# Optimization experiments

Measured on AMD Instinct MI355X. Metric: run time of the kernel, lower is better.

## Reference

```python
import jax, jax.numpy as jnp
import numpy as np
import math

PHI = (1.0 + math.sqrt(5.0)) / 2.0
BASE_FAST = PHI
BASE_SLOW = 1618.0
D = 1024
NH = 16
HD = D // NH
H_GATE = max(8, D // 4)
B, L = 2, 2048


def _rope_cos_sin(seq_len, dim, base):
    # dim assumed even here (D=1024)
    idx = jnp.arange(0, dim, 2, dtype=jnp.float32) / float(dim)
    inv = 1.0 / (base ** idx)
    t = jnp.arange(seq_len, dtype=jnp.float32)
    freqs = jnp.outer(t, inv)                      # (L, dim/2)
    emb = jnp.concatenate([freqs, freqs], axis=-1) # (L, dim)
    return jnp.cos(emb), jnp.sin(emb)


def _rotate_half(x):
    d = x.shape[-1]
    x1, x2 = x[..., : d // 2], x[..., d // 2 :]
    return jnp.concatenate([-x2, x1], axis=-1)


def setup_inputs() -> dict:
    key = jax.random.key(0)
    ks = jax.random.split(key, 16)
    std = 0.02
    inp = {
        "z": jax.random.normal(ks[0], (B, L, D), jnp.float32),
        "pool_seq": jax.random.normal(ks[1], (B, L, D), jnp.float32),
        "Wq": std * jax.random.normal(ks[2], (D, D), jnp.float32),
        "bq": jnp.zeros((D,), jnp.float32),
        "Wk": std * jax.random.normal(ks[3], (D, D), jnp.float32),
        "bk": jnp.zeros((D,), jnp.float32),
        "Wv": std * jax.random.normal(ks[4], (D, D), jnp.float32),
        "bv": jnp.zeros((D,), jnp.float32),
        "W_coh": std * jax.random.normal(ks[5], (D, D), jnp.float32),
        "gamma": jnp.zeros((1,), jnp.float32) + 0.1,  # nonzero so bias path is exercised
        "Wg1": std * jax.random.normal(ks[6], (H_GATE, D), jnp.float32),
        "bg1": jnp.zeros((H_GATE,), jnp.float32),
        "Wg2": std * jax.random.normal(ks[7], (1, H_GATE), jnp.float32),
        "bg2": jnp.zeros((1,), jnp.float32),
    }
    return inp


def reference(z, pool_seq, Wq, bq, Wk, bk, Wv, bv, W_coh, gamma, Wg1, bg1, Wg2, bg2):
    b, l, d = z.shape
    # QKV projections (torch Linear: x @ W^T + b)
    Q = z @ Wq.T + bq
    K_raw = z @ Wk.T + bk
    V = z @ Wv.T + bv

    # Global coherence bias: per-query pool vector dotted with every key
    gk = pool_seq @ W_coh.T                                   # (B,L,D)
    gb = jnp.einsum("bqd,bkd->bqk", gk, K_raw) * (d ** -0.5)  # (B,L,L)
    gb = jnp.tanh(gamma[0]) * gb

    # Per-position RoPE interpolation gate (exact GELU as in torch default)
    h = jax.nn.gelu(pool_seq @ Wg1.T + bg1, approximate=False)
    gate = jax.nn.sigmoid(h @ Wg2.T + bg2)                    # (B,L,1)

    cos_f, sin_f = _rope_cos_sin(l, d, BASE_FAST)             # (L,D)
    cos_s, sin_s = _rope_cos_sin(l, d, BASE_SLOW)
    cos = gate * cos_f + (1.0 - gate) * cos_s                 # (B,L,D)
    sin = gate * sin_f + (1.0 - gate) * sin_s

    Q = Q * cos + _rotate_half(Q) * sin
    K_rot = K_raw * cos + _rotate_half(K_raw) * sin

    nh, hd = NH, d // NH
    Q_h = Q.reshape(b, l, nh, hd).transpose(0, 2, 1, 3)       # (B,H,L,hd)
    K_h = K_rot.reshape(b, l, nh, hd).transpose(0, 2, 1, 3)
    V_h = V.reshape(b, l, nh, hd).transpose(0, 2, 1, 3)

    logits = jnp.einsum("bhqd,bhkd->bhqk", Q_h, K_h) * (hd ** -0.5)
    logits = logits + gb[:, None]                             # broadcast over heads

    causal = jnp.tril(jnp.ones((l, l), dtype=bool))
    logits = jnp.where(causal[None, None], logits, -jnp.inf)

    attn_w_h = jax.nn.softmax(logits, axis=-1)                # (B,H,L,L)
    out_h = jnp.einsum("bhqk,bhkd->bhqd", attn_w_h, V_h)
    out = out_h.transpose(0, 2, 1, 3).reshape(b, l, d)
    attn_w = attn_w_h.mean(axis=1)                            # (B,L,L)
    return out, attn_w
```

## Files before the change

kernel.cpp:

```cpp
#include <hip/hip_runtime.h>
#include <hip/hip_bf16.h>

constexpr int Bn  = 2;
constexpr int Ln  = 2048;
constexpr int Dn  = 1024;
constexpr int NH  = 16;
constexpr int HGn = 256;
constexpr long BLD = (long)Bn * Ln * Dn;

typedef float f32x4 __attribute__((ext_vector_type(4)));
typedef float f32x2 __attribute__((ext_vector_type(2)));
typedef short s16x8 __attribute__((ext_vector_type(8)));
typedef short s16x4 __attribute__((ext_vector_type(4)));
typedef short s16x2 __attribute__((ext_vector_type(2)));

#define DEVI static __device__ __forceinline__

DEVI float bf2f(short u) {
  union { float f; unsigned int i; } v; v.i = ((unsigned int)(unsigned short)u) << 16; return v.f;
}
DEVI short f2bf(float f) {
  union { float f; unsigned int i; } v; v.f = f;
  unsigned int r = v.i + 0x7FFFu + ((v.i >> 16) & 1u);
  return (short)(r >> 16);
}
DEVI void gl_lds16(const void* g, void* l) {
  __builtin_amdgcn_global_load_lds((const __attribute__((address_space(1))) unsigned int*)g,
                                   (__attribute__((address_space(3))) unsigned int*)l, 16, 0, 0);
}

struct CastDesc { const float* src[7]; long cum[8]; };
__global__ void k_cast7(CastDesc d, short* __restrict__ dst) {
  long gi = ((long)blockIdx.x * 256 + threadIdx.x) * 4;
  int s = 0;
#pragma unroll
  for (int i = 1; i < 7; ++i) if (gi >= d.cum[i]) s = i;
  const float* sp = d.src[s] + (gi - d.cum[s]);
  f32x4 v = *(const f32x4*)sp;
  s16x4 o; o[0] = f2bf(v[0]); o[1] = f2bf(v[1]); o[2] = f2bf(v[2]); o[3] = f2bf(v[3]);
  *(s16x4*)(dst + gi) = o;
}

__global__ __launch_bounds__(256)
void k_gemm_mega(const short* __restrict__ zb, const short* __restrict__ pb,
                 const short* __restrict__ Wcat,
                 const float* __restrict__ bq, const float* __restrict__ bk,
                 const float* __restrict__ bv, const float* __restrict__ bg1,
                 short* __restrict__ Qp, short* __restrict__ Kp,
                 short* __restrict__ Vtb, short* __restrict__ Gk,
                 float* __restrict__ Hf) {
  int m0 = blockIdx.y * 128, n0 = blockIdx.x * 128;
  const short* Ap = (n0 < 3072) ? zb : pb;
  __shared__ short smA[128 * 32];
  __shared__ short smB[128 * 32];
  int tid = threadIdx.x;
  int lane = tid & 63, wid = tid >> 6;
  int wr = wid >> 1, wc = wid & 1;
  int lr = lane & 15, lg = lane >> 4;
  int r_in = lane >> 2, c_in = (lane & 3) * 8;
  f32x4 acc[4][4] = {};
  for (int k0 = 0; k0 < Dn; k0 += 32) {
#pragma unroll
    for (int i = 0; i < 2; ++i) {
      int row = wid * 32 + i * 16 + r_in;
      gl_lds16(Ap + (long)(m0 + row) * Dn + k0 + c_in, smA + row * 32 + c_in);
      gl_lds16(Wcat + (long)(n0 + row) * Dn + k0 + c_in, smB + row * 32 + c_in);
    }
    __syncthreads();
    s16x8 af[4], bf[4];
#pragma unroll
    for (int m = 0; m < 4; m++) af[m] = *(const s16x8*)(smA + (wr * 64 + m * 16 + lr) * 32 + lg * 8);
#pragma unroll
    for (int n = 0; n < 4; n++) bf[n] = *(const s16x8*)(smB + (wc * 64 + n * 16 + lr) * 32 + lg * 8);
#pragma unroll
    for (int m = 0; m < 4; m++)
#pragma unroll
      for (int n = 0; n < 4; n++)
        acc[m][n] = __builtin_amdgcn_mfma_f32_16x16x32_bf16(af[m], bf[n], acc[m][n], 0, 0, 0);
    __syncthreads();
  }
  int slice = n0 >> 10;
#pragma unroll
  for (int n = 0; n < 4; n++) {
    int col = n0 + wc * 64 + n * 16 + lr;
    int c = col - (slice << 10);
    float bias = (slice == 0) ? bq[c] : (slice == 1) ? bk[c] : (slice == 2) ? bv[c]
               : (slice == 3) ? 0.0f : bg1[c];
#pragma unroll
    for (int m = 0; m < 4; m++) {
#pragma unroll
      for (int r = 0; r < 4; r++) {
        long row = m0 + wr * 64 + m * 16 + lg * 4 + r;
        float v = acc[m][n][r] + bias;
        if (slice == 4) {
          v = 0.5f * v * (1.0f + erff(v * 0.70710678118f));
          Hf[row * HGn + c] = v;
        } else if (slice == 2) {
          long off = (((row >> 11) * (long)NH + (c >> 6)) * 64 + (c & 63)) * Ln + (row & (Ln - 1));
          Vtb[off] = f2bf(v);
        } else {
          short* dst = (slice == 0) ? Qp : (slice == 1) ? Kp : Gk;
          dst[row * (long)Dn + c] = f2bf(v);
        }
      }
    }
  }
}

__global__ __launch_bounds__(256)
void k_gemm_gb(const short* __restrict__ A, const short* __restrict__ B,
               const float* __restrict__ gamma, short* __restrict__ C) {
  int bz = blockIdx.z;
  const short* Ap = A + (long)bz * Ln * Dn;
  const short* Bp = B + (long)bz * Ln * Dn;
  int m0 = blockIdx.y * 128, n0 = blockIdx.x * 128;
  if (n0 > m0 + 127) return;
  __shared__ short smA[128 * 32];
  __shared__ short smB[128 * 32];
  int tid = threadIdx.x;
  int lane = tid & 63, wid = tid >> 6;
  int wr = wid >> 1, wc = wid & 1;
  int lr = lane & 15, lg = lane >> 4;
  int r_in = lane >> 2, c_in = (lane & 3) * 8;
  f32x4 acc[4][4] = {};
  for (int k0 = 0; k0 < Dn; k0 += 32) {
#pragma unroll
    for (int i = 0; i < 2; ++i) {
      int row = wid * 32 + i * 16 + r_in;
      gl_lds16(Ap + (long)(m0 + row) * Dn + k0 + c_in, smA + row * 32 + c_in);
      gl_lds16(Bp + (long)(n0 + row) * Dn + k0 + c_in, smB + row * 32 + c_in);
    }
    __syncthreads();
    s16x8 af[4], bf[4];
#pragma unroll
    for (int m = 0; m < 4; m++) af[m] = *(const s16x8*)(smA + (wr * 64 + m * 16 + lr) * 32 + lg * 8);
#pragma unroll
    for (int n = 0; n < 4; n++) bf[n] = *(const s16x8*)(smB + (wc * 64 + n * 16 + lr) * 32 + lg * 8);
#pragma unroll
    for (int m = 0; m < 4; m++)
#pragma unroll
      for (int n = 0; n < 4; n++)
        acc[m][n] = __builtin_amdgcn_mfma_f32_16x16x32_bf16(af[m], bf[n], acc[m][n], 0, 0, 0);
    __syncthreads();
  }
  float alpha = tanhf(gamma[0]) * 0.03125f;
#pragma unroll
  for (int n = 0; n < 4; n++) {
    int col = n0 + wc * 64 + n * 16 + lr;
#pragma unroll
    for (int m = 0; m < 4; m++) {
#pragma unroll
      for (int r = 0; r < 4; r++) {
        long row = m0 + wr * 64 + m * 16 + lg * 4 + r;
        C[(long)bz * Ln * Ln + row * Ln + col] = f2bf(acc[m][n][r] * alpha);
      }
    }
  }
}

__global__ void k_rope_tables(float* __restrict__ ctf, float* __restrict__ stf,
                              float* __restrict__ cts, float* __restrict__ sts) {
  int idx = blockIdx.x * 256 + threadIdx.x;
  int l = idx >> 9, j = idx & 511;
  float e = (float)j * (1.0f / 512.0f);
  float invf = powf(1.6180339887498949f, -e);
  float invs = powf(1618.0f, -e);
  float af = (float)l * invf, as = (float)l * invs;
  float sf, cf, ss, cs;
  sincosf(af, &sf, &cf);
  sincosf(as, &ss, &cs);
  ctf[idx] = cf; stf[idx] = sf; cts[idx] = cs; sts[idx] = ss;
}

__global__ void k_gate(const float* __restrict__ Hf, const float* __restrict__ Wg2,
                       const float* __restrict__ bg2, float* __restrict__ gate) {
  int lane = threadIdx.x & 63, wid = threadIdx.x >> 6;
  int row = blockIdx.x * 4 + wid;
  f32x4 h = *(const f32x4*)(Hf + (long)row * HGn + lane * 4);
  f32x4 w = *(const f32x4*)(Wg2 + lane * 4);
  float s = h[0] * w[0] + h[1] * w[1] + h[2] * w[2] + h[3] * w[3];
#pragma unroll
  for (int m = 1; m < 64; m <<= 1) s += __shfl_xor(s, m);
  if (lane == 0) gate[row] = 1.0f / (1.0f + __expf(-(s + bg2[0])));
}

__global__ void k_rope(short* __restrict__ Q, short* __restrict__ Kx,
                       const float* __restrict__ gate,
                       const float* __restrict__ ctf, const float* __restrict__ stf,
                       const float* __restrict__ cts, const float* __restrict__ sts) {
  int bl = blockIdx.x;
  int l = bl & (Ln - 1);
  int t = threadIdx.x;
  float g = gate[bl];
  int j = t * 2;
  f32x2 vcf = *(const f32x2*)(ctf + l * 512 + j);
  f32x2 vsf = *(const f32x2*)(stf + l * 512 + j);
  f32x2 vcs = *(const f32x2*)(cts + l * 512 + j);
  f32x2 vss = *(const f32x2*)(sts + l * 512 + j);
  float c0 = g * vcf[0] + (1.f - g) * vcs[0];
  float c1 = g * vcf[1] + (1.f - g) * vcs[1];
  float s0 = g * vsf[0] + (1.f - g) * vss[0];
  float s1 = g * vsf[1] + (1.f - g) * vss[1];
  long base = (long)bl * Dn + j;
  {
    s16x2 xa = *(const s16x2*)(Q + base);
    s16x2 xb = *(const s16x2*)(Q + base + 512);
    float a0 = bf2f(xa[0]), a1 = bf2f(xa[1]), b0 = bf2f(xb[0]), b1 = bf2f(xb[1]);
    s16x2 o0, o1;
    o0[0] = f2bf(a0 * c0 - b0 * s0); o0[1] = f2bf(a1 * c1 - b1 * s1);
    o1[0] = f2bf(b0 * c0 + a0 * s0); o1[1] = f2bf(b1 * c1 + a1 * s1);
    *(s16x2*)(Q + base) = o0;
    *(s16x2*)(Q + base + 512) = o1;
  }
  {
    s16x2 xa = *(const s16x2*)(Kx + base);
    s16x2 xb = *(const s16x2*)(Kx + base + 512);
    float a0 = bf2f(xa[0]), a1 = bf2f(xa[1]), b0 = bf2f(xb[0]), b1 = bf2f(xb[1]);
    s16x2 o0, o1;
    o0[0] = f2bf(a0 * c0 - b0 * s0); o0[1] = f2bf(a1 * c1 - b1 * s1);
    o1[0] = f2bf(b0 * c0 + a0 * s0); o1[1] = f2bf(b1 * c1 + a1 * s1);
    *(s16x2*)(Kx + base) = o0;
    *(s16x2*)(Kx + base + 512) = o1;
  }
}

__global__ __launch_bounds__(256)
void k_attn1(const short* __restrict__ Q, const short* __restrict__ Kx,
             const short* __restrict__ Vt, const short* __restrict__ Gb,
             float* __restrict__ outp, float* __restrict__ zinv) {
  int wg = blockIdx.x;
  int xcd = wg & 7, slot = wg >> 3;
  int p = slot & 15, gh = slot >> 4;
  int g = gh * 8 + xcd;
  int b = g >> 4, h = g & 15;

  int tid = threadIdx.x;
  int lane = tid & 63, w = tid >> 6;
  int lr = lane & 15, lg = lane >> 4;
  __shared__ short smK[2][64 * 64];
  __shared__ short smV[2][64 * 64];
  __shared__ short smP[4 * 16 * 64];
  short* pw = smP + w * 1024;

  int r0 = w * 16 + (lane >> 3);
  int scol = ((lane & 7) ^ (lane >> 3)) * 8;
  const short* Kg = Kx + (long)(b * Ln) * Dn + h * 64;
  const short* Vg = Vt + (long)(b * NH + h) * 64 * Ln;
  int sw = (lr & 7) << 3;

  for (int seg = 0; seg < 2; ++seg) {
    int qb = seg ? (31 - p) : p;
    int q0w = qb * 64 + w * 16;
    const short* qbp = Q + ((long)(b * Ln) + q0w + lr) * Dn + h * 64 + lg * 8;
    s16x8 qf0 = *(const s16x8*)(qbp);
    s16x8 qf1 = *(const s16x8*)(qbp + 32);
    f32x4 acc[4] = {};
    float az[4] = {0.f, 0.f, 0.f, 0.f};
    const short* gbase = Gb + ((long)b * Ln + q0w + lg * 4) * Ln + lr;

    int nt = qb + 1;
    auto stage = [&](int buf, int t) {
      long k0 = (long)t * 64;
      short* bK = &smK[buf][w * 1024];
      short* bV = &smV[buf][w * 1024];
      gl_lds16(Kg + (k0 + r0) * Dn + scol,           bK);
      gl_lds16(Kg + (k0 + r0 + 8) * Dn + scol,       bK + 512);
      gl_lds16(Vg + (long)r0 * Ln + k0 + scol,       bV);
      gl_lds16(Vg + (long)(r0 + 8) * Ln + k0 + scol, bV + 512);
    };

    float gcur[4][4], gnxt[4][4];
    stage(0, 0);
    {
      const short* g0 = gbase;
#pragma unroll
      for (int kk = 0; kk < 4; ++kk)
#pragma unroll
        for (int r = 0; r < 4; ++r) gcur[kk][r] = bf2f(g0[(long)r * Ln + kk * 16]);
    }
    int cur = 0;
    for (int t = 0; t < nt; ++t) {
      bool pre = (t + 1 < nt);
      if (pre) {
        const short* g0 = gbase + (t + 1) * 64;
#pragma unroll
        for (int kk = 0; kk < 4; ++kk)
#pragma unroll
          for (int r = 0; r < 4; ++r) gnxt[kk][r] = bf2f(g0[(long)r * Ln + kk * 16]);
        stage(cur ^ 1, t + 1);
      }
      __builtin_amdgcn_sched_barrier(0);
      if (pre) asm volatile("s_waitcnt vmcnt(20)" ::: "memory");
      else     asm volatile("s_waitcnt vmcnt(0)" ::: "memory");
      __builtin_amdgcn_s_barrier();
      __builtin_amdgcn_sched_barrier(0);
      int k0 = t * 64;
      const short* Kc = smK[cur];
      const short* Vc = smV[cur];
#pragma unroll
      for (int kk = 0; kk < 4; ++kk) {
        const short* kr = Kc + (kk * 16 + lr) * 64;
        s16x8 kf0 = *(const s16x8*)(kr + ((lg * 8) ^ sw));
        s16x8 kf1 = *(const s16x8*)(kr + ((32 + lg * 8) ^ sw));
        f32x4 S = {};
        S = __builtin_amdgcn_mfma_f32_16x16x32_bf16(qf0, kf0, S, 0, 0, 0);
        S = __builtin_amdgcn_mfma_f32_16x16x32_bf16(qf1, kf1, S, 0, 0, 0);
        int k = k0 + kk * 16 + lr;
#pragma unroll
        for (int r = 0; r < 4; r++) {
          int q = q0w + lg * 4 + r;
          float arg = (k <= q) ? (S[r] * 0.125f + gcur[kk][r]) : -80.0f;
          float pv = __expf(arg);
          az[r] += pv;
          int qq = lg * 4 + r;
          pw[qq * 64 + ((kk * 16 + lr) ^ ((qq & 7) << 3))] = f2bf(pv);
        }
      }
#pragma unroll
      for (int c = 0; c < 2; ++c) {
        s16x8 pf = *(const s16x8*)(pw + lr * 64 + ((c * 32 + lg * 8) ^ sw));
#pragma unroll
        for (int n = 0; n < 4; n++) {
          s16x8 vf = *(const s16x8*)(Vc + (n * 16 + lr) * 64 + ((c * 32 + lg * 8) ^ sw));
          acc[n] = __builtin_amdgcn_mfma_f32_16x16x32_bf16(pf, vf, acc[n], 0, 0, 0);
        }
      }
      __builtin_amdgcn_s_barrier();
      if (pre) {
#pragma unroll
        for (int kk = 0; kk < 4; ++kk)
#pragma unroll
          for (int r = 0; r < 4; ++r) gcur[kk][r] = gnxt[kk][r];
      }
      cur ^= 1;
    }
#pragma unroll
    for (int r = 0; r < 4; r++) {
      float z = az[r];
      z += __shfl_xor(z, 1); z += __shfl_xor(z, 2); z += __shfl_xor(z, 4); z += __shfl_xor(z, 8);
      az[r] = 1.0f / z;
    }
    if (lr == 0) {
#pragma unroll
      for (int r = 0; r < 4; r++)
        zinv[((long)(b * NH + h)) * Ln + q0w + lg * 4 + r] = az[r];
    }
#pragma unroll
    for (int n = 0; n < 4; n++) {
#pragma unroll
      for (int r = 0; r < 4; r++) {
        int q = q0w + lg * 4 + r;
        outp[((long)(b * Ln) + q) * Dn + h * 64 + n * 16 + lr] = acc[n][r] * az[r];
      }
    }
  }
}

__global__ __launch_bounds__(256)
void k_attn2(const short* __restrict__ Qm, const short* __restrict__ Kx,
             const short* __restrict__ Gb, const float* __restrict__ zinv, float* __restrict__ aw) {
  int b = blockIdx.y;
  int t = blockIdx.x;
  int qb = t >> 5, kb = t & 31;
  int q0 = qb * 64, k0 = kb * 64;
  int tid = threadIdx.x;
  if (kb > qb) {
    int row = tid >> 2, c4 = (tid & 3) << 4;
    float* basep = aw + ((long)b * Ln + q0 + row) * Ln + k0 + c4;
    f32x4 z = {};
    *(f32x4*)(basep) = z; *(f32x4*)(basep + 4) = z;
    *(f32x4*)(basep + 8) = z; *(f32x4*)(basep + 12) = z;
    return;
  }
  int lane = tid & 63, w = tid >> 6;
  int lr = lane & 15, lg = lane >> 4;
  int q0w = q0 + w * 16;
  bool diag = (qb == kb);
  __shared__ short smK[2][64 * 64];
  __shared__ short smQ[2][64 * 64];
  __shared__ float smZ[NH * 64];
  for (int i = tid; i < NH * 64; i += 256) {
    int h = i >> 6, qq = i & 63;
    smZ[i] = zinv[((long)(b * NH + h)) * Ln + q0 + qq];
  }
  __syncthreads();
  float gv[4][4];
#pragma unroll
  for (int n = 0; n < 4; n++) {
    int k = k0 + n * 16 + lr;
#pragma unroll
    for (int r = 0; r < 4; r++)
      gv[n][r] = bf2f(Gb[((long)b * Ln + q0w + lg * 4 + r) * Ln + k]);
  }
  int r0 = w * 16 + (lane >> 3);
  int scol = ((lane & 7) ^ (lane >> 3)) * 8;
  int sw = (lr & 7) << 3;
  auto stage = [&](int buf, int h) {
    short* bK = &smK[buf][w * 1024];
    short* bQ = &smQ[buf][w * 1024];
    const short* Kg = Kx + ((long)(b * Ln) + k0 + r0) * Dn + h * 64 + scol;
    gl_lds16(Kg, bK);
    gl_lds16(Kg + 8 * Dn, bK + 512);
    const short* Qg = Qm + ((long)(b * Ln) + q0 + r0) * Dn + h * 64 + scol;
    gl_lds16(Qg, bQ);
    gl_lds16(Qg + 8 * Dn, bQ + 512);
  };
  float wa[4][4] = {{0.f}};
  stage(0, 0);
  int cur = 0;
  for (int h = 0; h < NH; ++h) {
    bool pre = (h + 1 < NH);
    if (pre) stage(cur ^ 1, h + 1);
    __builtin_amdgcn_sched_barrier(0);
    if (pre) asm volatile("s_waitcnt vmcnt(4)" ::: "memory");
    else     asm volatile("s_waitcnt vmcnt(0)" ::: "memory");
    __builtin_amdgcn_s_barrier();
    __builtin_amdgcn_sched_barrier(0);
    const short* Kc = smK[cur];
    const short* Qc = smQ[cur];
    s16x8 qf0 = *(const s16x8*)(Qc + (w * 16 + lr) * 64 + ((lg * 8) ^ sw));
    s16x8 qf1 = *(const s16x8*)(Qc + (w * 16 + lr) * 64 + ((32 + lg * 8) ^ sw));
    float zq[4];
#pragma unroll
    for (int r = 0; r < 4; r++) zq[r] = smZ[h * 64 + w * 16 + lg * 4 + r];
#pragma unroll
    for (int n = 0; n < 4; n++) {
      const short* kr = Kc + (n * 16 + lr) * 64;
      s16x8 kf0 = *(const s16x8*)(kr + ((lg * 8) ^ sw));
      s16x8 kf1 = *(const s16x8*)(kr + ((32 + lg * 8) ^ sw));
      f32x4 S = {};
      S = __builtin_amdgcn_mfma_f32_16x16x32_bf16(qf0, kf0, S, 0, 0, 0);
      S = __builtin_amdgcn_mfma_f32_16x16x32_bf16(qf1, kf1, S, 0, 0, 0);
#pragma unroll
      for (int r = 0; r < 4; r++)
        wa[n][r] += __expf(S[r] * 0.125f + gv[n][r]) * zq[r];
    }
    __builtin_amdgcn_s_barrier();
    cur ^= 1;
  }
#pragma unroll
  for (int n = 0; n < 4; n++) {
    int k = k0 + n * 16 + lr;
#pragma unroll
    for (int r = 0; r < 4; r++) {
      int q = q0w + lg * 4 + r;
      float v = wa[n][r] * (1.0f / 16.0f);
      if (diag && k > q) v = 0.0f;
      aw[((long)b * Ln + q) * Ln + k] = v;
    }
  }
}

extern "C" void kernel_launch(void* const* d_in, const int* in_sizes, int n_in,
                              void* d_out, int out_size, void* d_ws, size_t ws_size,
                              hipStream_t stream) {
  const float* z    = (const float*)d_in[0];
  const float* ps   = (const float*)d_in[1];
  const float* Wq   = (const float*)d_in[2];
  const float* bq   = (const float*)d_in[3];
  const float* Wk   = (const float*)d_in[4];
  const float* bk   = (const float*)d_in[5];
  const float* Wv   = (const float*)d_in[6];
  const float* bv   = (const float*)d_in[7];
  const float* Wc   = (const float*)d_in[8];
  const float* gamma= (const float*)d_in[9];
  const float* Wg1  = (const float*)d_in[10];
  const float* bg1  = (const float*)d_in[11];
  const float* Wg2  = (const float*)d_in[12];
  const float* bg2  = (const float*)d_in[13];

  char* w = (char*)d_ws;
  auto alloc = [&](long bytes) { void* p = (void*)w; w += (bytes + 255) & ~255L; return p; };
  short* zb   = (short*)alloc(BLD * 2);
  short* pb   = (short*)alloc(BLD * 2);
  short* Wcat = (short*)alloc((long)(4 * Dn + HGn) * Dn * 2);
  short* Qp   = (short*)alloc(BLD * 2);
  short* Kp   = (short*)alloc(BLD * 2);
  short* Vtb  = (short*)alloc(BLD * 2);
  short* Gk   = (short*)alloc(BLD * 2);
  float* Hf   = (float*)alloc((long)Bn * Ln * HGn * 4);
  float* gate = (float*)alloc((long)Bn * Ln * 4);
  float* ctf  = (float*)alloc((long)Ln * 512 * 4);
  float* stf  = (float*)alloc((long)Ln * 512 * 4);
  float* cts  = (float*)alloc((long)Ln * 512 * 4);
  float* sts  = (float*)alloc((long)Ln * 512 * 4);
  float* zv   = (float*)alloc((long)Bn * NH * Ln * 4);
  short* Gb   = (short*)zb;

  float* outp = (float*)d_out;
  float* aw   = outp + BLD;

  CastDesc cd;
  cd.src[0] = z;  cd.src[1] = ps; cd.src[2] = Wq; cd.src[3] = Wk;
  cd.src[4] = Wv; cd.src[5] = Wc; cd.src[6] = Wg1;
  long c0 = 0;
  cd.cum[0] = 0;
  cd.cum[1] = (c0 += BLD);
  cd.cum[2] = (c0 += BLD);
  cd.cum[3] = (c0 += (long)Dn * Dn);
  cd.cum[4] = (c0 += (long)Dn * Dn);
  cd.cum[5] = (c0 += (long)Dn * Dn);
  cd.cum[6] = (c0 += (long)Dn * Dn);
  cd.cum[7] = (c0 += (long)HGn * Dn);
  k_cast7<<<(int)(c0 / 1024), 256, 0, stream>>>(cd, zb);

  k_gemm_mega<<<dim3((4 * Dn + HGn) / 128, (Bn * Ln) / 128), 256, 0, stream>>>(
      zb, pb, Wcat, bq, bk, bv, bg1, Qp, Kp, Vtb, Gk, Hf);

  k_gemm_gb<<<dim3(Ln / 128, Ln / 128, Bn), 256, 0, stream>>>(Gk, Kp, gamma, Gb);

  k_rope_tables<<<(Ln * 512) / 256, 256, 0, stream>>>(ctf, stf, cts, sts);
  k_gate<<<(Bn * Ln) / 4, 256, 0, stream>>>(Hf, Wg2, bg2, gate);
  k_rope<<<Bn * Ln, 256, 0, stream>>>(Qp, Kp, gate, ctf, stf, cts, sts);

  k_attn1<<<512, 256, 0, stream>>>(Qp, Kp, Vtb, Gb, outp, zv);
  k_attn2<<<dim3(32 * 32, Bn), 256, 0, stream>>>(Qp, Kp, Gb, zv, aw);
}
```

Baseline: 251.5 us.

## Double-buffer GEMM LDS tiles with swizzle, block remap and triangular grid

```diff
diff --git a/kernel.cpp b/kernel.cpp
--- a/kernel.cpp
+++ b/kernel.cpp
@@ -49,35 +49,52 @@
                  short* __restrict__ Qp, short* __restrict__ Kp,
                  short* __restrict__ Vtb, short* __restrict__ Gk,
                  float* __restrict__ Hf) {
-  int m0 = blockIdx.y * 128, n0 = blockIdx.x * 128;
+  int lin = blockIdx.y * 34 + blockIdx.x;
+  int id2 = (lin & 7) * 136 + (lin >> 3);
+  int n0 = (id2 % 34) * 128, m0 = (id2 / 34) * 128;
   const short* Ap = (n0 < 3072) ? zb : pb;
-  __shared__ short smA[128 * 32];
-  __shared__ short smB[128 * 32];
+  __shared__ short smA[2][128 * 32];
+  __shared__ short smB[2][128 * 32];
   int tid = threadIdx.x;
   int lane = tid & 63, wid = tid >> 6;
   int wr = wid >> 1, wc = wid & 1;
   int lr = lane & 15, lg = lane >> 4;
-  int r_in = lane >> 2, c_in = (lane & 3) * 8;
+  int r_in = lane >> 2;
+  int slot = (lane & 3) * 8;
+  int scol = ((lane & 3) ^ ((lane >> 3) & 3)) * 8;
+  int rsw = (lr >> 1) & 3;
   f32x4 acc[4][4] = {};
+  auto stage = [&](int buf, int k0) {
+    int rowA = wid * 32 + r_in;
+    gl_lds16(Ap   + (long)(m0 + rowA)      * Dn + k0 + scol, &smA[buf][rowA * 32 + slot]);
+    gl_lds16(Ap   + (long)(m0 + rowA + 16) * Dn + k0 + scol, &smA[buf][(rowA + 16) * 32 + slot]);
+    gl_lds16(Wcat + (long)(n0 + rowA)      * Dn + k0 + scol, &smB[buf][rowA * 32 + slot]);
+    gl_lds16(Wcat + (long)(n0 + rowA + 16) * Dn + k0 + scol, &smB[buf][(rowA + 16) * 32 + slot]);
+  };
+  stage(0, 0);
+  int cur = 0;
   for (int k0 = 0; k0 < Dn; k0 += 32) {
-#pragma unroll
-    for (int i = 0; i < 2; ++i) {
-      int row = wid * 32 + i * 16 + r_in;
-      gl_lds16(Ap + (long)(m0 + row) * Dn + k0 + c_in, smA + row * 32 + c_in);
-      gl_lds16(Wcat + (long)(n0 + row) * Dn + k0 + c_in, smB + row * 32 + c_in);
-    }
-    __syncthreads();
+    bool pre = (k0 + 32 < Dn);
+    if (pre) stage(cur ^ 1, k0 + 32);
+    __builtin_amdgcn_sched_barrier(0);
+    if (pre) asm volatile("s_waitcnt vmcnt(4)" ::: "memory");
+    else     asm volatile("s_waitcnt vmcnt(0)" ::: "memory");
+    __builtin_amdgcn_s_barrier();
+    __builtin_amdgcn_sched_barrier(0);
     s16x8 af[4], bf[4];
 #pragma unroll
-    for (int m = 0; m < 4; m++) af[m] = *(const s16x8*)(smA + (wr * 64 + m * 16 + lr) * 32 + lg * 8);
-#pragma unroll
-    for (int n = 0; n < 4; n++) bf[n] = *(const s16x8*)(smB + (wc * 64 + n * 16 + lr) * 32 + lg * 8);
+    for (int m = 0; m < 4; m++)
+      af[m] = *(const s16x8*)(&smA[cur][(wr * 64 + m * 16 + lr) * 32 + ((lg ^ rsw) * 8)]);
+#pragma unroll
+    for (int n = 0; n < 4; n++)
+      bf[n] = *(const s16x8*)(&smB[cur][(wc * 64 + n * 16 + lr) * 32 + ((lg ^ rsw) * 8)]);
 #pragma unroll
     for (int m = 0; m < 4; m++)
 #pragma unroll
       for (int n = 0; n < 4; n++)
         acc[m][n] = __builtin_amdgcn_mfma_f32_16x16x32_bf16(af[m], bf[n], acc[m][n], 0, 0, 0);
-    __syncthreads();
+    __builtin_amdgcn_s_barrier();
+    cur ^= 1;
   }
   int slice = n0 >> 10;
 #pragma unroll
@@ -110,38 +127,57 @@
 __global__ __launch_bounds__(256)
 void k_gemm_gb(const short* __restrict__ A, const short* __restrict__ B,
                const float* __restrict__ gamma, short* __restrict__ C) {
-  int bz = blockIdx.z;
+  int bz = blockIdx.y;
+  int t = blockIdx.x;
+  int qb = (int)((sqrtf(8.0f * (float)t + 1.0f) - 1.0f) * 0.5f);
+  while ((qb + 1) * (qb + 2) / 2 <= t) ++qb;
+  while (qb * (qb + 1) / 2 > t) --qb;
+  int kb = t - qb * (qb + 1) / 2;
+  int m0 = qb * 128, n0 = kb * 128;
   const short* Ap = A + (long)bz * Ln * Dn;
   const short* Bp = B + (long)bz * Ln * Dn;
-  int m0 = blockIdx.y * 128, n0 = blockIdx.x * 128;
-  if (n0 > m0 + 127) return;
-  __shared__ short smA[128 * 32];
-  __shared__ short smB[128 * 32];
+  __shared__ short smA[2][128 * 32];
+  __shared__ short smB[2][128 * 32];
   int tid = threadIdx.x;
   int lane = tid & 63, wid = tid >> 6;
   int wr = wid >> 1, wc = wid & 1;
   int lr = lane & 15, lg = lane >> 4;
-  int r_in = lane >> 2, c_in = (lane & 3) * 8;
+  int r_in = lane >> 2;
+  int slot = (lane & 3) * 8;
+  int scol = ((lane & 3) ^ ((lane >> 3) & 3)) * 8;
+  int rsw = (lr >> 1) & 3;
   f32x4 acc[4][4] = {};
+  auto stage = [&](int buf, int k0) {
+    int rowA = wid * 32 + r_in;
+    gl_lds16(Ap + (long)(m0 + rowA)      * Dn + k0 + scol, &smA[buf][rowA * 32 + slot]);
+    gl_lds16(Ap + (long)(m0 + rowA + 16) * Dn + k0 + scol, &smA[buf][(rowA + 16) * 32 + slot]);
+    gl_lds16(Bp + (long)(n0 + rowA)      * Dn + k0 + scol, &smB[buf][rowA * 32 + slot]);
+    gl_lds16(Bp + (long)(n0 + rowA + 16) * Dn + k0 + scol, &smB[buf][(rowA + 16) * 32 + slot]);
+  };
+  stage(0, 0);
+  int cur = 0;
   for (int k0 = 0; k0 < Dn; k0 += 32) {
-#pragma unroll
-    for (int i = 0; i < 2; ++i) {
-      int row = wid * 32 + i * 16 + r_in;
-      gl_lds16(Ap + (long)(m0 + row) * Dn + k0 + c_in, smA + row * 32 + c_in);
-      gl_lds16(Bp + (long)(n0 + row) * Dn + k0 + c_in, smB + row * 32 + c_in);
-    }
-    __syncthreads();
+    bool pre = (k0 + 32 < Dn);
+    if (pre) stage(cur ^ 1, k0 + 32);
+    __builtin_amdgcn_sched_barrier(0);
+    if (pre) asm volatile("s_waitcnt vmcnt(4)" ::: "memory");
+    else     asm volatile("s_waitcnt vmcnt(0)" ::: "memory");
+    __builtin_amdgcn_s_barrier();
+    __builtin_amdgcn_sched_barrier(0);
     s16x8 af[4], bf[4];
 #pragma unroll
-    for (int m = 0; m < 4; m++) af[m] = *(const s16x8*)(smA + (wr * 64 + m * 16 + lr) * 32 + lg * 8);
-#pragma unroll
-    for (int n = 0; n < 4; n++) bf[n] = *(const s16x8*)(smB + (wc * 64 + n * 16 + lr) * 32 + lg * 8);
+    for (int m = 0; m < 4; m++)
+      af[m] = *(const s16x8*)(&smA[cur][(wr * 64 + m * 16 + lr) * 32 + ((lg ^ rsw) * 8)]);
+#pragma unroll
+    for (int n = 0; n < 4; n++)
+      bf[n] = *(const s16x8*)(&smB[cur][(wc * 64 + n * 16 + lr) * 32 + ((lg ^ rsw) * 8)]);
 #pragma unroll
     for (int m = 0; m < 4; m++)
 #pragma unroll
       for (int n = 0; n < 4; n++)
         acc[m][n] = __builtin_amdgcn_mfma_f32_16x16x32_bf16(af[m], bf[n], acc[m][n], 0, 0, 0);
-    __syncthreads();
+    __builtin_amdgcn_s_barrier();
+    cur ^= 1;
   }
   float alpha = tanhf(gamma[0]) * 0.03125f;
 #pragma unroll
@@ -507,7 +543,7 @@
   k_gemm_mega<<<dim3((4 * Dn + HGn) / 128, (Bn * Ln) / 128), 256, 0, stream>>>(
       zb, pb, Wcat, bq, bk, bv, bg1, Qp, Kp, Vtb, Gk, Hf);
 
-  k_gemm_gb<<<dim3(Ln / 128, Ln / 128, Bn), 256, 0, stream>>>(Gk, Kp, gamma, Gb);
+  k_gemm_gb<<<dim3(16 * 17 / 2, Bn), 256, 0, stream>>>(Gk, Kp, gamma, Gb);
 
   k_rope_tables<<<(Ln * 512) / 256, 256, 0, stream>>>(ctf, stf, cts, sts);
   k_gate<<<(Bn * Ln) / 4, 256, 0, stream>>>(Hf, Wg2, bg2, gate);
```

Result: no change. 249.0 us (-1.0%).

## Rewrite projection and bias GEMMs as 256x256 double-buffered 8-wave kernels

Applied to the files above, without the earlier changes.

```diff
diff --git a/kernel.cpp b/kernel.cpp
--- a/kernel.cpp
+++ b/kernel.cpp
@@ -41,118 +41,152 @@
   *(s16x4*)(dst + gi) = o;
 }
 
-__global__ __launch_bounds__(256)
-void k_gemm_mega(const short* __restrict__ zb, const short* __restrict__ pb,
-                 const short* __restrict__ Wcat,
-                 const float* __restrict__ bq, const float* __restrict__ bk,
-                 const float* __restrict__ bv, const float* __restrict__ bg1,
-                 short* __restrict__ Qp, short* __restrict__ Kp,
-                 short* __restrict__ Vtb, short* __restrict__ Gk,
-                 float* __restrict__ Hf) {
-  int m0 = blockIdx.y * 128, n0 = blockIdx.x * 128;
-  const short* Ap = (n0 < 3072) ? zb : pb;
-  __shared__ short smA[128 * 32];
-  __shared__ short smB[128 * 32];
+template<int MODE>
+__global__ __launch_bounds__(512)
+void k_gemm8(const short* __restrict__ Aall, const short* __restrict__ Ball,
+             const short* __restrict__ Wcat,
+             const float* __restrict__ bq, const float* __restrict__ bk,
+             const float* __restrict__ bv, const float* __restrict__ bg1,
+             short* __restrict__ Qp, short* __restrict__ Kp,
+             short* __restrict__ Vtb, short* __restrict__ Gk,
+             float* __restrict__ Hf,
+             const float* __restrict__ gamma, short* __restrict__ Gb) {
+  int m0, n0;
+  const short* Ap; const short* Bp;
+  long cbase = 0;
+  if (MODE == 0) {
+    int wgid = blockIdx.x;
+    int xcd = wgid & 7, idx = wgid >> 3;
+    n0 = (idx >> 1) * 256;
+    m0 = (xcd * 2 + (idx & 1)) * 256;
+    Ap = (n0 < 3072) ? Aall : Ball;
+    Bp = Wcat;
+  } else {
+    int tt = blockIdx.x;
+    int bz = (tt >= 36) ? 1 : 0; int t6 = tt - bz * 36;
+    int qb = 0;
+    while ((qb + 1) * (qb + 2) / 2 <= t6) ++qb;
+    int kb = t6 - qb * (qb + 1) / 2;
+    m0 = qb * 256; n0 = kb * 256;
+    Ap = Aall + (long)bz * Ln * Dn;
+    Bp = Ball + (long)bz * Ln * Dn;
+    cbase = (long)bz * Ln * Ln;
+  }
+  __shared__ short smA[2][2][128 * 64];
+  __shared__ short smB[2][2][128 * 64];
   int tid = threadIdx.x;
-  int lane = tid & 63, wid = tid >> 6;
-  int wr = wid >> 1, wc = wid & 1;
+  int lane = tid & 63, w = tid >> 6;
+  int wr = w >> 2, wc = w & 3;
   int lr = lane & 15, lg = lane >> 4;
-  int r_in = lane >> 2, c_in = (lane & 3) * 8;
-  f32x4 acc[4][4] = {};
-  for (int k0 = 0; k0 < Dn; k0 += 32) {
-#pragma unroll
-    for (int i = 0; i < 2; ++i) {
-      int row = wid * 32 + i * 16 + r_in;
-      gl_lds16(Ap + (long)(m0 + row) * Dn + k0 + c_in, smA + row * 32 + c_in);
-      gl_lds16(Wcat + (long)(n0 + row) * Dn + k0 + c_in, smB + row * 32 + c_in);
-    }
-    __syncthreads();
-    s16x8 af[4], bf[4];
-#pragma unroll
-    for (int m = 0; m < 4; m++) af[m] = *(const s16x8*)(smA + (wr * 64 + m * 16 + lr) * 32 + lg * 8);
-#pragma unroll
-    for (int n = 0; n < 4; n++) bf[n] = *(const s16x8*)(smB + (wc * 64 + n * 16 + lr) * 32 + lg * 8);
-#pragma unroll
-    for (int m = 0; m < 4; m++)
-#pragma unroll
-      for (int n = 0; n < 4; n++)
-        acc[m][n] = __builtin_amdgcn_mfma_f32_16x16x32_bf16(af[m], bf[n], acc[m][n], 0, 0, 0);
-    __syncthreads();
-  }
-  int slice = n0 >> 10;
-#pragma unroll
-  for (int n = 0; n < 4; n++) {
-    int col = n0 + wc * 64 + n * 16 + lr;
-    int c = col - (slice << 10);
-    float bias = (slice == 0) ? bq[c] : (slice == 1) ? bk[c] : (slice == 2) ? bv[c]
-               : (slice == 3) ? 0.0f : bg1[c];
-#pragma unroll
-    for (int m = 0; m < 4; m++) {
-#pragma unroll
-      for (int r = 0; r < 4; r++) {
-        long row = m0 + wr * 64 + m * 16 + lg * 4 + r;
-        float v = acc[m][n][r] + bias;
-        if (slice == 4) {
-          v = 0.5f * v * (1.0f + erff(v * 0.70710678118f));
-          Hf[row * HGn + c] = v;
-        } else if (slice == 2) {
-          long off = (((row >> 11) * (long)NH + (c >> 6)) * 64 + (c & 63)) * Ln + (row & (Ln - 1));
-          Vtb[off] = f2bf(v);
-        } else {
-          short* dst = (slice == 0) ? Qp : (slice == 1) ? Kp : Gk;
-          dst[row * (long)Dn + c] = f2bf(v);
+  int srow = lane >> 3;
+  int scol = ((lane & 7) ^ (lane >> 3)) * 8;
+  f32x4 acc[8][4] = {};
+
+  auto stage_half = [&](int d, int q, int t) {
+    int x = q & 1;
+    const short* base = (q < 2) ? (Ap + (long)(m0 + x * 128) * Dn)
+                                : (Bp + (long)(n0 + x * 128) * Dn);
+    short* dst = (q < 2) ? &smA[d][x][0] : &smB[d][x][0];
+#pragma unroll
+    for (int j = 0; j < 2; ++j)
+      gl_lds16(base + (long)((j * 8 + w) * 8 + srow) * Dn + t * 64 + scol,
+               dst + (j * 8 + w) * 512);
+  };
+
+  auto phase = [&](int d, int q, int stq, int stt, int sd, bool doStage, bool sync) {
+    int qm = q & 1, qn = q >> 1;
+    const short* Ah = &smA[d][wr][0];
+    const short* Bh = &smB[d][wc >> 1][0];
+    s16x8 af[2][4], bf[2][2];
+#pragma unroll
+    for (int ks = 0; ks < 2; ++ks) {
+#pragma unroll
+      for (int m = 0; m < 4; ++m) {
+        int row = (qm * 4 + m) * 16 + lr;
+        af[ks][m] = *(const s16x8*)(Ah + row * 64 + (((ks * 4 + lg) ^ (lr & 7)) * 8));
+      }
+#pragma unroll
+      for (int n = 0; n < 2; ++n) {
+        int row = (wc & 1) * 64 + (qn * 2 + n) * 16 + lr;
+        bf[ks][n] = *(const s16x8*)(Bh + row * 64 + (((ks * 4 + lg) ^ (lr & 7)) * 8));
+      }
+    }
+    if (doStage) stage_half(sd, stq, stt);
+    __builtin_amdgcn_sched_barrier(0);
+    if (sync) asm volatile("s_waitcnt vmcnt(0)" ::: "memory");
+    __builtin_amdgcn_s_barrier();
+    asm volatile("s_waitcnt lgkmcnt(0)" ::: "memory");
+    __builtin_amdgcn_sched_barrier(0);
+    __builtin_amdgcn_s_setprio(1);
+#pragma unroll
+    for (int ks = 0; ks < 2; ++ks)
+#pragma unroll
+      for (int m = 0; m < 4; ++m)
+#pragma unroll
+        for (int n = 0; n < 2; ++n)
+          acc[qm * 4 + m][qn * 2 + n] = __builtin_amdgcn_mfma_f32_16x16x32_bf16(
+              af[ks][m], bf[ks][n], acc[qm * 4 + m][qn * 2 + n], 0, 0, 0);
+    __builtin_amdgcn_s_setprio(0);
+    __builtin_amdgcn_sched_barrier(0);
+    __builtin_amdgcn_s_barrier();
+  };
+
+#pragma unroll
+  for (int q = 0; q < 4; ++q) stage_half(0, q, 0);
+  asm volatile("s_waitcnt vmcnt(0)" ::: "memory");
+  __builtin_amdgcn_s_barrier();
+
+  for (int i = 0; i < 8; ++i) {
+    phase(0, 0, 0, 2 * i + 1, 1, true, false);
+    phase(0, 1, 1, 2 * i + 1, 1, true, false);
+    phase(0, 2, 2, 2 * i + 1, 1, true, false);
+    phase(0, 3, 3, 2 * i + 1, 1, true, true);
+    bool more = (i < 7);
+    phase(1, 0, 0, 2 * i + 2, 0, more, false);
+    phase(1, 1, 1, 2 * i + 2, 0, more, false);
+    phase(1, 2, 2, 2 * i + 2, 0, more, false);
+    phase(1, 3, 3, 2 * i + 2, 0, more, true);
+  }
+
+  if (MODE == 0) {
+    int slice = n0 >> 10;
+#pragma unroll
+    for (int n = 0; n < 4; n++) {
+      int col = n0 + wc * 64 + n * 16 + lr;
+      int c = col - (slice << 10);
+      float bias = (slice == 0) ? bq[c] : (slice == 1) ? bk[c] : (slice == 2) ? bv[c]
+                 : (slice == 3) ? 0.0f : bg1[c];
+#pragma unroll
+      for (int m = 0; m < 8; m++) {
+#pragma unroll
+        for (int r = 0; r < 4; r++) {
+          long row = m0 + wr * 128 + m * 16 + lg * 4 + r;
+          float v = acc[m][n][r] + bias;
+          if (slice == 4) {
+            v = 0.5f * v * (1.0f + erff(v * 0.70710678118f));
+            Hf[row * HGn + c] = v;
+          } else if (slice == 2) {
+            long off = (((row >> 11) * (long)NH + (c >> 6)) * 64 + (c & 63)) * Ln + (row & (Ln - 1));
+            Vtb[off] = f2bf(v);
+          } else {
+            short* dst = (slice == 0) ? Qp : (slice == 1) ? Kp : Gk;
+            dst[row * (long)Dn + c] = f2bf(v);
+          }
         }
       }
     }
-  }
-}
-
-__global__ __launch_bounds__(256)
-void k_gemm_gb(const short* __restrict__ A, const short* __restrict__ B,
-               const float* __restrict__ gamma, short* __restrict__ C) {
-  int bz = blockIdx.z;
-  const short* Ap = A + (long)bz * Ln * Dn;
-  const short* Bp = B + (long)bz * Ln * Dn;
-  int m0 = blockIdx.y * 128, n0 = blockIdx.x * 128;
-  if (n0 > m0 + 127) return;
-  __shared__ short smA[128 * 32];
-  __shared__ short smB[128 * 32];
-  int tid = threadIdx.x;
-  int lane = tid & 63, wid = tid >> 6;
-  int wr = wid >> 1, wc = wid & 1;
-  int lr = lane & 15, lg = lane >> 4;
-  int r_in = lane >> 2, c_in = (lane & 3) * 8;
-  f32x4 acc[4][4] = {};
-  for (int k0 = 0; k0 < Dn; k0 += 32) {
-#pragma unroll
-    for (int i = 0; i < 2; ++i) {
-      int row = wid * 32 + i * 16 + r_in;
-      gl_lds16(Ap + (long)(m0 + row) * Dn + k0 + c_in, smA + row * 32 + c_in);
-      gl_lds16(Bp + (long)(n0 + row) * Dn + k0 + c_in, smB + row * 32 + c_in);
-    }
-    __syncthreads();
-    s16x8 af[4], bf[4];
-#pragma unroll
-    for (int m = 0; m < 4; m++) af[m] = *(const s16x8*)(smA + (wr * 64 + m * 16 + lr) * 32 + lg * 8);
-#pragma unroll
-    for (int n = 0; n < 4; n++) bf[n] = *(const s16x8*)(smB + (wc * 64 + n * 16 + lr) * 32 + lg * 8);
-#pragma unroll
-    for (int m = 0; m < 4; m++)
-#pragma unroll
-      for (int n = 0; n < 4; n++)
-        acc[m][n] = __builtin_amdgcn_mfma_f32_16x16x32_bf16(af[m], bf[n], acc[m][n], 0, 0, 0);
-    __syncthreads();
-  }
-  float alpha = tanhf(gamma[0]) * 0.03125f;
-#pragma unroll
-  for (int n = 0; n < 4; n++) {
-    int col = n0 + wc * 64 + n * 16 + lr;
-#pragma unroll
-    for (int m = 0; m < 4; m++) {
-#pragma unroll
-      for (int r = 0; r < 4; r++) {
-        long row = m0 + wr * 64 + m * 16 + lg * 4 + r;
-        C[(long)bz * Ln * Ln + row * Ln + col] = f2bf(acc[m][n][r] * alpha);
+  } else {
+    float alpha = tanhf(gamma[0]) * 0.03125f;
+#pragma unroll
+    for (int n = 0; n < 4; n++) {
+      int col = n0 + wc * 64 + n * 16 + lr;
+#pragma unroll
+      for (int m = 0; m < 8; m++) {
+#pragma unroll
+        for (int r = 0; r < 4; r++) {
+          long row = m0 + wr * 128 + m * 16 + lg * 4 + r;
+          Gb[cbase + row * Ln + col] = f2bf(acc[m][n][r] * alpha);
+        }
       }
     }
   }
@@ -504,10 +538,11 @@
   cd.cum[7] = (c0 += (long)HGn * Dn);
   k_cast7<<<(int)(c0 / 1024), 256, 0, stream>>>(cd, zb);
 
-  k_gemm_mega<<<dim3((4 * Dn + HGn) / 128, (Bn * Ln) / 128), 256, 0, stream>>>(
-      zb, pb, Wcat, bq, bk, bv, bg1, Qp, Kp, Vtb, Gk, Hf);
-
-  k_gemm_gb<<<dim3(Ln / 128, Ln / 128, Bn), 256, 0, stream>>>(Gk, Kp, gamma, Gb);
+  k_gemm8<0><<<272, 512, 0, stream>>>(zb, pb, Wcat, bq, bk, bv, bg1,
+                                      Qp, Kp, Vtb, Gk, Hf, nullptr, nullptr);
+
+  k_gemm8<1><<<72, 512, 0, stream>>>(Gk, Kp, nullptr, nullptr, nullptr, nullptr, nullptr,
+                                     nullptr, nullptr, nullptr, nullptr, nullptr, gamma, Gb);
 
   k_rope_tables<<<(Ln * 512) / 256, 256, 0, stream>>>(ctf, stf, cts, sts);
   k_gate<<<(Bn * Ln) / 4, 256, 0, stream>>>(Hf, Wg2, bg2, gate);
```

Result: slower. 360.5 us (+43.4%).
